# Optimization experiments

Measured on AMD Instinct MI355X. Metric: run time of the kernel, lower is better.

## Reference

```python
import jax, jax.numpy as jnp
import numpy as np

N_FFT = 4096
HOP = 1024
MAX_FRAMES = 345  # 44100*8 // 1024 + 1
BATCH = 8


def _build_buffers():
    N = N_FFT
    half = N // 2
    n = np.arange(N)
    k = np.arange(half + 1)
    ang = 2.0 * np.pi * np.outer(k, n) / N
    # fourier_basis = [real(fft(eye)[:half+1]); imag(fft(eye)[:half+1])], W[k,n]=exp(-2pi i kn/N)
    F = np.vstack([np.cos(ang), -np.sin(ang)])  # [N+2, N], float64
    window = 0.5 - 0.5 * np.cos(2.0 * np.pi * n / N)  # periodic hann, max == 1.0
    # rows of F are mutually orthogonal -> pinv(F) = F.T @ diag(1/||row||^2) (zero rows -> 0)
    norms = np.sum(F ** 2, axis=1)
    inv_norm = np.where(norms > 1e-6, 1.0 / norms, 0.0)
    # inverse_basis = window * pinv(F * N/HOP).T * sqrt(N)   (normalized=True)
    scale = inv_norm * (HOP / N) * np.sqrt(N)
    inverse_basis = (window[None, :] * F * scale[:, None]).astype(np.float32)  # [N+2, N]
    # window_sum normalization buffer
    T = MAX_FRAMES
    n_len = N + HOP * (T - 1)
    win_sq = (window / np.abs(window).max()) ** 2
    window_sum = np.zeros(n_len, dtype=np.float64)
    for i in range(T):
        s = i * HOP
        window_sum[s:s + N] += win_sq
    window_sum_inv = (N / (window_sum * HOP + 1e-8)).astype(np.float32)  # [n_len]
    return jnp.asarray(inverse_basis), jnp.asarray(window_sum_inv)


def setup_inputs() -> dict:
    key = jax.random.key(0)
    k1, k2 = jax.random.split(key)
    real = jax.random.normal(k1, (BATCH, N_FFT // 2 + 1, MAX_FRAMES), dtype=jnp.float32)
    imag = jax.random.normal(k2, (BATCH, N_FFT // 2 + 1, MAX_FRAMES), dtype=jnp.float32)
    inverse_basis, window_sum_inv = _build_buffers()
    return {"real": real, "imag": imag, "inverse_basis": inverse_basis,
            "window_sum_inv": window_sum_inv, "length": 352800}


def reference(real, imag, inverse_basis, window_sum_inv, length):
    eps = jnp.finfo(real.dtype).eps
    magnitude = jnp.sqrt(real ** 2 + imag ** 2)
    phase = jnp.arctan2(imag, real + eps)
    # [B, N+2, T]
    complex_input = jnp.concatenate([magnitude * jnp.cos(phase),
                                     magnitude * jnp.sin(phase)], axis=1)
    # conv_transpose1d(stride=HOP) == per-frame IDFT matmul + overlap-add
    frames = jnp.einsum('bct,ck->btk', complex_input, inverse_basis)  # [B, T, N]
    B, T, K = frames.shape
    n_len = K + HOP * (T - 1)
    idx = (jnp.arange(T)[:, None] * HOP + jnp.arange(K)[None, :]).reshape(-1)
    sig = jnp.zeros((B, n_len), frames.dtype).at[:, idx].add(frames.reshape(B, -1))
    half = K // 2
    out = sig[:, half:] * window_sum_inv[half:n_len]  # [B, n_len - half]
    if length:
        pad = max(0, length - out.shape[-1])
        out = jnp.pad(out, ((0, 0), (0, pad)))[:, :length]
    return out
```

## Files before the change

kernel.cpp:

```cpp
#include <hip/hip_runtime.h>
#include <cstdint>
#include <cstddef>

#define B_SZ  8
#define C_IN  2049
#define T_FR  345
#define NFFT  4096
#define HOPSZ 1024
#define MFR   2760
#define TW    1.5339807878856412e-3f

typedef float f4 __attribute__((ext_vector_type(4)));

__device__ __forceinline__ unsigned short f2b(float f) {
  union { float f; unsigned int u; } v; v.f = f;
  unsigned int r = v.u + 0x7fffu + ((v.u >> 16) & 1u);
  return (unsigned short)(r >> 16);
}
__device__ __forceinline__ float b2f(unsigned int h) {
  union { unsigned int u; float f; } v; v.u = h << 16;
  return v.f;
}

__global__ void trans(const float* __restrict__ re, const float* __restrict__ im,
                      unsigned int* __restrict__ spec) {
  __shared__ float tr[64][65];
  __shared__ float ti[64][65];
  const int tid = threadIdx.x;
  const int t0 = blockIdx.x * 64;
  const int c0 = blockIdx.y * 64;
  const int b  = blockIdx.z;
#pragma unroll
  for (int pass = 0; pass < 16; ++pass) {
    int idx = pass * 256 + tid;
    int tt = idx & 63, cc = idx >> 6;
    int c = c0 + cc, t = t0 + tt;
    float rp = 0.f, ip = 0.f;
    if (c < C_IN && t < T_FR) {
      size_t off = ((size_t)b * C_IN + c) * T_FR + t;
      float r = re[off], i = im[off];
      float x   = r + 1.1920929e-7f;
      float mag = sqrtf(r * r + i * i);
      float h2  = sqrtf(x * x + i * i);
      float inv = (h2 > 0.f) ? (mag / h2) : 0.f;
      rp = x * inv;
      ip = i * inv;
    }
    tr[cc][tt] = rp;
    ti[cc][tt] = ip;
  }
  __syncthreads();
#pragma unroll
  for (int pass = 0; pass < 16; ++pass) {
    int idx = pass * 256 + tid;
    int kk = idx & 63, tt = idx >> 6;
    int c = c0 + kk, t = t0 + tt;
    if (c < C_IN && t < T_FR) {
      size_t mrow = (size_t)b * T_FR + t;
      unsigned int pk = ((unsigned int)f2b(ti[kk][tt]) << 16) | f2b(tr[kk][tt]);
      spec[mrow * C_IN + c] = pk;
    }
  }
}

template<int M, int L2M>
__device__ __forceinline__ void fft_stage(const f4* __restrict__ sr, const f4* __restrict__ si,
                                          f4* __restrict__ dr, f4* __restrict__ di, int tid) {
  f4 ar = sr[tid],       ai = si[tid];
  f4 br = sr[tid + 256], bi = si[tid + 256];
  f4 cr = sr[tid + 512], ci = si[tid + 512];
  f4 er = sr[tid + 768], ei = si[tid + 768];
  f4 t0r = ar + cr, t0i = ai + ci;
  f4 t1r = ar - cr, t1i = ai - ci;
  f4 t2r = br + er, t2i = bi + ei;
  f4 t3r = ei - bi, t3i = br - er;
  f4 y0r = t0r + t2r, y0i = t0i + t2i;
  f4 u1r = t1r + t3r, u1i = t1i + t3i;
  f4 u2r = t0r - t2r, u2i = t0i - t2i;
  f4 u3r = t1r - t3r, u3i = t1i - t3i;
  const int base = tid << 2;
  if (M == 1) {
#pragma unroll
    for (int p = 0; p < 4; ++p) {
      int j = base + p;
      float s1, c1; __sincosf((float)j * TW, &s1, &c1);
      float c2 = c1 * c1 - s1 * s1, s2 = 2.f * c1 * s1;
      float c3 = c2 * c1 - s2 * s1, s3 = s2 * c1 + c2 * s1;
      f4 o, oi;
      o.x  = y0r[p];
      o.y  = c1 * u1r[p] - s1 * u1i[p];
      o.z  = c2 * u2r[p] - s2 * u2i[p];
      o.w  = c3 * u3r[p] - s3 * u3i[p];
      oi.x = y0i[p];
      oi.y = c1 * u1i[p] + s1 * u1r[p];
      oi.z = c2 * u2i[p] + s2 * u2r[p];
      oi.w = c3 * u3i[p] + s3 * u3r[p];
      dr[j] = o; di[j] = oi;
    }
  } else {
    const int j  = base >> L2M;
    const int kb = (base & (M - 1)) >> 2;
    float s1, c1; __sincosf((float)(j * M) * TW, &s1, &c1);
    float c2 = c1 * c1 - s1 * s1, s2 = 2.f * c1 * s1;
    float c3 = c2 * c1 - s2 * s1, s3 = s2 * c1 + c2 * s1;
    const int wb = kb + M * j;
    const int Q  = M >> 2;
    dr[wb]         = y0r;                      di[wb]         = y0i;
    dr[wb + Q]     = c1 * u1r - s1 * u1i;      di[wb + Q]     = c1 * u1i + s1 * u1r;
    dr[wb + 2 * Q] = c2 * u2r - s2 * u2i;      di[wb + 2 * Q] = c2 * u2i + s2 * u2r;
    dr[wb + 3 * Q] = c3 * u3r - s3 * u3i;      di[wb + 3 * Q] = c3 * u3i + s3 * u3r;
  }
}

__global__ __launch_bounds__(256) void ifft_frames(const unsigned int* __restrict__ spec,
                                                   unsigned short* __restrict__ Fr) {
  __shared__ f4 B0r[1024], B0i[1024], B1r[1024], B1i[1024];
  float* r0 = (float*)B0r;
  float* i0 = (float*)B0i;
  const int m = blockIdx.x, tid = threadIdx.x;
  const unsigned int* sp = spec + (size_t)m * C_IN;
#pragma unroll
  for (int p = 0; p < 8; ++p) {
    int k = p * 256 + tid;
    unsigned int v = sp[k];
    float a = b2f(v & 0xffffu), b = b2f(v >> 16);
    r0[k] = a; i0[k] = b;
    if (k >= 1) { r0[4096 - k] = a; i0[4096 - k] = -b; }
  }
  if (tid == 0) {
    unsigned int v = sp[2048];
    r0[2048] = b2f(v & 0xffffu); i0[2048] = b2f(v >> 16);
  }
  __syncthreads();
  fft_stage<1,    0>(B0r, B0i, B1r, B1i, tid); __syncthreads();
  fft_stage<4,    2>(B1r, B1i, B0r, B0i, tid); __syncthreads();
  fft_stage<16,   4>(B0r, B0i, B1r, B1i, tid); __syncthreads();
  fft_stage<64,   6>(B1r, B1i, B0r, B0i, tid); __syncthreads();
  fft_stage<256,  8>(B0r, B0i, B1r, B1i, tid); __syncthreads();
  fft_stage<1024,10>(B1r, B1i, B0r, B0i, tid); __syncthreads();
  unsigned short* dst = Fr + (size_t)m * NFFT;
#pragma unroll
  for (int p = 0; p < 16; ++p) {
    int n = p * 256 + tid;
    float w = (0.5f - 0.5f * __cosf((float)n * TW)) * 0.00390625f;
    dst[n] = f2b(r0[n] * w);
  }
}

__global__ void ola(const unsigned short* __restrict__ Fr, const float* __restrict__ wsi,
                    float* __restrict__ out, int length) {
  int p = blockIdx.x * 256 + threadIdx.x;
  int b = blockIdx.y;
  if (p >= length) return;
  int s = (NFFT / 2) + p;
  int tlo = (s - 3072) >> 10;
  tlo = tlo < 0 ? 0 : tlo;
  int thi = s >> 10;
  thi = thi > (T_FR - 1) ? (T_FR - 1) : thi;
  float acc = 0.f;
  for (int t = tlo; t <= thi; ++t) {
    int n = s - (t << 10);
    acc += b2f((unsigned int)Fr[((size_t)(b * T_FR + t)) * NFFT + n]);
  }
  out[(size_t)b * length + p] = acc * wsi[s];
}

extern "C" void kernel_launch(void* const* d_in, const int* in_sizes, int n_in,
                              void* d_out, int out_size, void* d_ws, size_t ws_size,
                              hipStream_t stream) {
  const float* re  = (const float*)d_in[0];
  const float* im  = (const float*)d_in[1];
  const float* wsi = (const float*)d_in[3];
  float* out = (float*)d_out;
  const int length = out_size / B_SZ;

  unsigned int*   spec = (unsigned int*)d_ws;
  unsigned short* Fr   = (unsigned short*)(spec + (size_t)MFR * C_IN);

  trans<<<dim3((T_FR + 63) / 64, (C_IN + 63) / 64, B_SZ), 256, 0, stream>>>(re, im, spec);
  ifft_frames<<<dim3(MFR), 256, 0, stream>>>(spec, Fr);
  ola<<<dim3((length + 255) / 256, B_SZ), 256, 0, stream>>>(Fr, wsi, out, length);
}
```

Before: 197.4 us.

## Pack two real frames per complex IFFT and vectorize OLA and output stores

```diff
diff --git a/kernel.cpp b/kernel.cpp
--- a/kernel.cpp
+++ b/kernel.cpp
@@ -8,6 +8,7 @@
 #define NFFT  4096
 #define HOPSZ 1024
 #define MFR   2760
+#define NPAIR 173
 #define TW    1.5339807878856412e-3f
 
 typedef float f4 __attribute__((ext_vector_type(4)));
@@ -39,10 +40,10 @@
     if (c < C_IN && t < T_FR) {
       size_t off = ((size_t)b * C_IN + c) * T_FR + t;
       float r = re[off], i = im[off];
-      float x   = r + 1.1920929e-7f;
-      float mag = sqrtf(r * r + i * i);
-      float h2  = sqrtf(x * x + i * i);
-      float inv = (h2 > 0.f) ? (mag / h2) : 0.f;
+      float x  = r + 1.1920929e-7f;
+      float r2 = r * r + i * i;
+      float h2 = fmaxf(x * x + i * i, 1e-35f);
+      float inv = __builtin_amdgcn_sqrtf(r2) * __builtin_amdgcn_rsqf(h2);
       rp = x * inv;
       ip = i * inv;
     }
@@ -117,19 +118,31 @@
   __shared__ f4 B0r[1024], B0i[1024], B1r[1024], B1i[1024];
   float* r0 = (float*)B0r;
   float* i0 = (float*)B0i;
-  const int m = blockIdx.x, tid = threadIdx.x;
-  const unsigned int* sp = spec + (size_t)m * C_IN;
+  const int tid = threadIdx.x;
+  const int j = blockIdx.x, b = blockIdx.y;
+  const int ta = b * T_FR + 2 * j;
+  const bool hasb = (2 * j + 1) < T_FR;
+  const unsigned int* spa = spec + (size_t)ta * C_IN;
+  const unsigned int* spb = spa + C_IN;
 #pragma unroll
   for (int p = 0; p < 8; ++p) {
     int k = p * 256 + tid;
-    unsigned int v = sp[k];
-    float a = b2f(v & 0xffffu), b = b2f(v >> 16);
-    r0[k] = a; i0[k] = b;
-    if (k >= 1) { r0[4096 - k] = a; i0[4096 - k] = -b; }
+    unsigned int va = spa[k];
+    unsigned int vb = hasb ? spb[k] : 0u;
+    float ar = b2f(va & 0xffffu), ai = b2f(va >> 16);
+    float br = b2f(vb & 0xffffu), bi = b2f(vb >> 16);
+    if (k == 0) {
+      r0[0] = ar; i0[0] = br;
+    } else {
+      r0[k] = ar - bi;        i0[k] = ai + br;
+      r0[4096 - k] = ar + bi; i0[4096 - k] = br - ai;
+    }
   }
   if (tid == 0) {
-    unsigned int v = sp[2048];
-    r0[2048] = b2f(v & 0xffffu); i0[2048] = b2f(v >> 16);
+    unsigned int va = spa[2048];
+    unsigned int vb = hasb ? spb[2048] : 0u;
+    r0[2048] = b2f(va & 0xffffu);
+    i0[2048] = b2f(vb & 0xffffu);
   }
   __syncthreads();
   fft_stage<1,    0>(B0r, B0i, B1r, B1i, tid); __syncthreads();
@@ -138,31 +151,40 @@
   fft_stage<64,   6>(B1r, B1i, B0r, B0i, tid); __syncthreads();
   fft_stage<256,  8>(B0r, B0i, B1r, B1i, tid); __syncthreads();
   fft_stage<1024,10>(B1r, B1i, B0r, B0i, tid); __syncthreads();
-  unsigned short* dst = Fr + (size_t)m * NFFT;
-#pragma unroll
-  for (int p = 0; p < 16; ++p) {
-    int n = p * 256 + tid;
-    float w = (0.5f - 0.5f * __cosf((float)n * TW)) * 0.00390625f;
-    dst[n] = f2b(r0[n] * w);
+  unsigned int* da = (unsigned int*)(Fr + (size_t)ta * NFFT);
+  unsigned int* db = (unsigned int*)(Fr + (size_t)(ta + 1) * NFFT);
+#pragma unroll
+  for (int p = 0; p < 8; ++p) {
+    int n2 = p * 256 + tid;
+    int n = n2 * 2;
+    float w0 = (0.5f - 0.5f * __cosf((float)n * TW)) * 0.00390625f;
+    float w1 = (0.5f - 0.5f * __cosf((float)(n + 1) * TW)) * 0.00390625f;
+    da[n2] = ((unsigned int)f2b(r0[n + 1] * w1) << 16) | f2b(r0[n] * w0);
+    if (hasb)
+      db[n2] = ((unsigned int)f2b(i0[n + 1] * w1) << 16) | f2b(i0[n] * w0);
   }
 }
 
 __global__ void ola(const unsigned short* __restrict__ Fr, const float* __restrict__ wsi,
                     float* __restrict__ out, int length) {
-  int p = blockIdx.x * 256 + threadIdx.x;
+  int q = blockIdx.x * 256 + threadIdx.x;
   int b = blockIdx.y;
-  if (p >= length) return;
-  int s = (NFFT / 2) + p;
-  int tlo = (s - 3072) >> 10;
+  int p4 = q * 4;
+  if (p4 >= length) return;
+  int s0 = (NFFT / 2) + p4;
+  int tlo = (s0 - 3072) >> 10;
   tlo = tlo < 0 ? 0 : tlo;
-  int thi = s >> 10;
+  int thi = s0 >> 10;
   thi = thi > (T_FR - 1) ? (T_FR - 1) : thi;
-  float acc = 0.f;
+  float a0 = 0.f, a1 = 0.f, a2 = 0.f, a3 = 0.f;
   for (int t = tlo; t <= thi; ++t) {
-    int n = s - (t << 10);
-    acc += b2f((unsigned int)Fr[((size_t)(b * T_FR + t)) * NFFT + n]);
-  }
-  out[(size_t)b * length + p] = acc * wsi[s];
+    const unsigned short* fp = Fr + ((size_t)(b * T_FR + t)) * NFFT + (s0 - (t << 10));
+    ushort4 v = *(const ushort4*)fp;
+    a0 += b2f(v.x); a1 += b2f(v.y); a2 += b2f(v.z); a3 += b2f(v.w);
+  }
+  float4 wv = *(const float4*)(wsi + s0);
+  float4 o; o.x = a0 * wv.x; o.y = a1 * wv.y; o.z = a2 * wv.z; o.w = a3 * wv.w;
+  *(float4*)(out + (size_t)b * length + p4) = o;
 }
 
 extern "C" void kernel_launch(void* const* d_in, const int* in_sizes, int n_in,
@@ -178,6 +200,6 @@
   unsigned short* Fr   = (unsigned short*)(spec + (size_t)MFR * C_IN);
 
   trans<<<dim3((T_FR + 63) / 64, (C_IN + 63) / 64, B_SZ), 256, 0, stream>>>(re, im, spec);
-  ifft_frames<<<dim3(MFR), 256, 0, stream>>>(spec, Fr);
-  ola<<<dim3((length + 255) / 256, B_SZ), 256, 0, stream>>>(Fr, wsi, out, length);
-}
+  ifft_frames<<<dim3(NPAIR, B_SZ), 256, 0, stream>>>(spec, Fr);
+  ola<<<dim3((length / 4 + 255) / 256, B_SZ), 256, 0, stream>>>(Fr, wsi, out, length);
+}
```

Result: faster. 181.3 us (-8.1%).
